# Kernel optimization log

Measured on AMD Instinct MI355X. Metric: run time of the kernel, lower is better.

Reference implementation:

```python
import jax, jax.numpy as jnp
import numpy as np

LN_EPS = 1e-5


def setup_inputs() -> dict:
    key = jax.random.key(0)
    ks = jax.random.split(key, 5)
    B, P, C, D = 8192, 25, 256, 5
    return {
        "features": jax.random.normal(ks[0], (B, P, C), dtype=jnp.float32),
        "weights": jax.random.normal(ks[1], (P, C, C), dtype=jnp.float32) * 0.05,
        "bias": jax.random.normal(ks[2], (P, C), dtype=jnp.float32) * 0.05,
        "ln_gamma": jnp.ones((C,), dtype=jnp.float32),
        "ln_beta": jnp.zeros((C,), dtype=jnp.float32),
        "lin_w": jax.random.normal(ks[3], (D, C), dtype=jnp.float32) * 0.05,
        "lin_b": jnp.zeros((D,), dtype=jnp.float32),
    }


def reference(features, weights, bias, ln_gamma, ln_beta, lin_w, lin_b):
    # Torch: (features.unsqueeze(-1) * weights).sum(-1) + bias
    # Broadcast [B,P,C,1]*[P,C,C] then sum over last axis reduces the SAME
    # broadcast axis, so it equals features * row-sums of weights (per point).
    w_rowsum = jnp.sum(weights, axis=-1)            # [P, C]
    point_wise = features * w_rowsum + bias          # [B, P, C]
    # LayerNorm over the channel dim
    mu = jnp.mean(point_wise, axis=-1, keepdims=True)
    var = jnp.mean(jnp.square(point_wise - mu), axis=-1, keepdims=True)
    pw_norm = (point_wise - mu) * jax.lax.rsqrt(var + LN_EPS)
    pw_norm = pw_norm * ln_gamma + ln_beta
    # residual + ReLU + final linear
    h = jax.nn.relu(features + pw_norm)              # [B, P, C]
    return jnp.einsum("bpc,dc->bpd", h, lin_w) + lin_b  # [B, P, D]
```

## Files before the change

kernel.cpp:

```cpp
#include <hip/hip_runtime.h>

#define LN_EPS 1e-5f

__global__ __launch_bounds__(256) void wrowsum_kernel(
    const float* __restrict__ w, float* __restrict__ wr, int n_rows) {
  const int lane = threadIdx.x & 63;
  const int wv   = threadIdx.x >> 6;
  const int rc   = blockIdx.x * 4 + wv;
  if (rc >= n_rows) return;
  const float4 v = reinterpret_cast<const float4*>(w)[(size_t)rc * 64 + lane];
  float s = v.x + v.y + v.z + v.w;
#pragma unroll
  for (int off = 32; off; off >>= 1) s += __shfl_xor(s, off);
  if (lane == 0) wr[rc] = s;
}

__global__ __launch_bounds__(256) void fused_main(
    const float* __restrict__ features,
    const float* __restrict__ wrow,
    const float* __restrict__ bias,
    const float* __restrict__ gamma,
    const float* __restrict__ beta,
    const float* __restrict__ lin_w,
    const float* __restrict__ lin_b,
    float* __restrict__ out,
    int n_rows, int P) {
  const int lane = threadIdx.x & 63;
  const int wv   = threadIdx.x >> 6;
  const int r    = blockIdx.x * 4 + wv;
  if (r >= n_rows) return;
  const int p = r % P;

  const float4 f  = reinterpret_cast<const float4*>(features)[(size_t)r * 64 + lane];
  const float4 wr = reinterpret_cast<const float4*>(wrow + (size_t)p * 256)[lane];
  const float4 bs = reinterpret_cast<const float4*>(bias + (size_t)p * 256)[lane];
  const float4 g  = reinterpret_cast<const float4*>(gamma)[lane];
  const float4 bt = reinterpret_cast<const float4*>(beta)[lane];

  const float pw0 = fmaf(f.x, wr.x, bs.x);
  const float pw1 = fmaf(f.y, wr.y, bs.y);
  const float pw2 = fmaf(f.z, wr.z, bs.z);
  const float pw3 = fmaf(f.w, wr.w, bs.w);

  float s1 = (pw0 + pw1) + (pw2 + pw3);
  float s2 = fmaf(pw0, pw0, fmaf(pw1, pw1, fmaf(pw2, pw2, pw3 * pw3)));
#pragma unroll
  for (int off = 32; off; off >>= 1) {
    s1 += __shfl_xor(s1, off);
    s2 += __shfl_xor(s2, off);
  }
  const float mu  = s1 * (1.0f / 256.0f);
  const float var = fmaf(-mu, mu, s2 * (1.0f / 256.0f));
  const float inv = rsqrtf(var + LN_EPS);

  const float h0 = fmaxf(fmaf((pw0 - mu) * inv, g.x, bt.x) + f.x, 0.0f);
  const float h1 = fmaxf(fmaf((pw1 - mu) * inv, g.y, bt.y) + f.y, 0.0f);
  const float h2 = fmaxf(fmaf((pw2 - mu) * inv, g.z, bt.z) + f.z, 0.0f);
  const float h3 = fmaxf(fmaf((pw3 - mu) * inv, g.w, bt.w) + f.w, 0.0f);

  float acc[5];
#pragma unroll
  for (int d = 0; d < 5; ++d) {
    const float4 lw = reinterpret_cast<const float4*>(lin_w + d * 256)[lane];
    acc[d] = fmaf(h0, lw.x, fmaf(h1, lw.y, fmaf(h2, lw.z, h3 * lw.w)));
  }
#pragma unroll
  for (int off = 32; off; off >>= 1) {
#pragma unroll
    for (int d = 0; d < 5; ++d) acc[d] += __shfl_xor(acc[d], off);
  }

  if (lane < 5) {
    float v;
    switch (lane) {
      case 0:  v = acc[0]; break;
      case 1:  v = acc[1]; break;
      case 2:  v = acc[2]; break;
      case 3:  v = acc[3]; break;
      default: v = acc[4]; break;
    }
    out[(size_t)r * 5 + lane] = v + lin_b[lane];
  }
}

extern "C" void kernel_launch(void* const* d_in, const int* in_sizes, int n_in,
                              void* d_out, int out_size, void* d_ws, size_t ws_size,
                              hipStream_t stream) {
  const float* features = (const float*)d_in[0];
  const float* weights  = (const float*)d_in[1];
  const float* bias     = (const float*)d_in[2];
  const float* gamma    = (const float*)d_in[3];
  const float* beta     = (const float*)d_in[4];
  const float* lin_w    = (const float*)d_in[5];
  const float* lin_b    = (const float*)d_in[6];
  float* out = (float*)d_out;

  const int C  = 256;
  const int PC = in_sizes[2];
  const int P  = PC / C;
  const int BP = in_sizes[0] / C;

  float* wr = (float*)d_ws;

  wrowsum_kernel<<<(PC + 3) / 4, 256, 0, stream>>>(weights, wr, PC);

  fused_main<<<(BP + 3) / 4, 256, 0, stream>>>(
      features, wr, bias, gamma, beta, lin_w, lin_b, out, BP, P);
}
```

Measured before the change: 325.0 us.

## Process four rows per wavefront with 16-lane subgroups and shorter reductions

Each 64-lane wavefront now handles four rows, with 16 lanes per row and each lane loading four float4 chunks. Cross-lane reductions for the LayerNorm statistics and the final linear drop from six shuffle steps to four, and the grid shrinks by four. The aim is to cut shuffle and reduction overhead and raise memory-level parallelism per thread, at the cost of more registers per thread.

```diff
diff --git a/kernel.cpp b/kernel.cpp
--- a/kernel.cpp
+++ b/kernel.cpp
@@ -27,25 +27,46 @@
     int n_rows, int P) {
   const int lane = threadIdx.x & 63;
   const int wv   = threadIdx.x >> 6;
-  const int r    = blockIdx.x * 4 + wv;
+  const int sub  = lane & 15;
+  const int rg   = lane >> 4;
+  const int r    = blockIdx.x * 16 + wv * 4 + rg;
   if (r >= n_rows) return;
   const int p = r % P;
 
-  const float4 f  = reinterpret_cast<const float4*>(features)[(size_t)r * 64 + lane];
-  const float4 wr = reinterpret_cast<const float4*>(wrow + (size_t)p * 256)[lane];
-  const float4 bs = reinterpret_cast<const float4*>(bias + (size_t)p * 256)[lane];
-  const float4 g  = reinterpret_cast<const float4*>(gamma)[lane];
-  const float4 bt = reinterpret_cast<const float4*>(beta)[lane];
+  const float4* __restrict__ f4  = reinterpret_cast<const float4*>(features);
+  const float4* __restrict__ w4  = reinterpret_cast<const float4*>(wrow);
+  const float4* __restrict__ b4  = reinterpret_cast<const float4*>(bias);
+  const float4* __restrict__ g4  = reinterpret_cast<const float4*>(gamma);
+  const float4* __restrict__ t4  = reinterpret_cast<const float4*>(beta);
+  const float4* __restrict__ l4  = reinterpret_cast<const float4*>(lin_w);
 
-  const float pw0 = fmaf(f.x, wr.x, bs.x);
-  const float pw1 = fmaf(f.y, wr.y, bs.y);
-  const float pw2 = fmaf(f.z, wr.z, bs.z);
-  const float pw3 = fmaf(f.w, wr.w, bs.w);
+  float4 f[4], wr[4], bs[4], g[4], bt[4];
+#pragma unroll
+  for (int i = 0; i < 4; ++i) {
+    const int c4 = i * 16 + sub;
+    f[i]  = f4[(size_t)r * 64 + c4];
+    wr[i] = w4[(size_t)p * 64 + c4];
+    bs[i] = b4[(size_t)p * 64 + c4];
+    g[i]  = g4[c4];
+    bt[i] = t4[c4];
+  }
 
-  float s1 = (pw0 + pw1) + (pw2 + pw3);
-  float s2 = fmaf(pw0, pw0, fmaf(pw1, pw1, fmaf(pw2, pw2, pw3 * pw3)));
+  float4 pw[4];
+  float s1 = 0.0f, s2 = 0.0f;
 #pragma unroll
-  for (int off = 32; off; off >>= 1) {
+  for (int i = 0; i < 4; ++i) {
+    pw[i].x = fmaf(f[i].x, wr[i].x, bs[i].x);
+    pw[i].y = fmaf(f[i].y, wr[i].y, bs[i].y);
+    pw[i].z = fmaf(f[i].z, wr[i].z, bs[i].z);
+    pw[i].w = fmaf(f[i].w, wr[i].w, bs[i].w);
+    s1 += (pw[i].x + pw[i].y) + (pw[i].z + pw[i].w);
+    s2 = fmaf(pw[i].x, pw[i].x, s2);
+    s2 = fmaf(pw[i].y, pw[i].y, s2);
+    s2 = fmaf(pw[i].z, pw[i].z, s2);
+    s2 = fmaf(pw[i].w, pw[i].w, s2);
+  }
+#pragma unroll
+  for (int off = 8; off; off >>= 1) {
     s1 += __shfl_xor(s1, off);
     s2 += __shfl_xor(s2, off);
   }
@@ -53,33 +74,45 @@
   const float var = fmaf(-mu, mu, s2 * (1.0f / 256.0f));
   const float inv = rsqrtf(var + LN_EPS);
 
-  const float h0 = fmaxf(fmaf((pw0 - mu) * inv, g.x, bt.x) + f.x, 0.0f);
-  const float h1 = fmaxf(fmaf((pw1 - mu) * inv, g.y, bt.y) + f.y, 0.0f);
-  const float h2 = fmaxf(fmaf((pw2 - mu) * inv, g.z, bt.z) + f.z, 0.0f);
-  const float h3 = fmaxf(fmaf((pw3 - mu) * inv, g.w, bt.w) + f.w, 0.0f);
+  float4 h[4];
+#pragma unroll
+  for (int i = 0; i < 4; ++i) {
+    h[i].x = fmaxf(fmaf((pw[i].x - mu) * inv, g[i].x, bt[i].x) + f[i].x, 0.0f);
+    h[i].y = fmaxf(fmaf((pw[i].y - mu) * inv, g[i].y, bt[i].y) + f[i].y, 0.0f);
+    h[i].z = fmaxf(fmaf((pw[i].z - mu) * inv, g[i].z, bt[i].z) + f[i].z, 0.0f);
+    h[i].w = fmaxf(fmaf((pw[i].w - mu) * inv, g[i].w, bt[i].w) + f[i].w, 0.0f);
+  }
 
   float acc[5];
 #pragma unroll
   for (int d = 0; d < 5; ++d) {
-    const float4 lw = reinterpret_cast<const float4*>(lin_w + d * 256)[lane];
-    acc[d] = fmaf(h0, lw.x, fmaf(h1, lw.y, fmaf(h2, lw.z, h3 * lw.w)));
+    float a = 0.0f;
+#pragma unroll
+    for (int i = 0; i < 4; ++i) {
+      const float4 lw = l4[d * 64 + i * 16 + sub];
+      a = fmaf(h[i].x, lw.x, a);
+      a = fmaf(h[i].y, lw.y, a);
+      a = fmaf(h[i].z, lw.z, a);
+      a = fmaf(h[i].w, lw.w, a);
+    }
+    acc[d] = a;
   }
 #pragma unroll
-  for (int off = 32; off; off >>= 1) {
+  for (int off = 8; off; off >>= 1) {
 #pragma unroll
     for (int d = 0; d < 5; ++d) acc[d] += __shfl_xor(acc[d], off);
   }
 
-  if (lane < 5) {
+  if (sub < 5) {
     float v;
-    switch (lane) {
+    switch (sub) {
       case 0:  v = acc[0]; break;
       case 1:  v = acc[1]; break;
       case 2:  v = acc[2]; break;
       case 3:  v = acc[3]; break;
       default: v = acc[4]; break;
     }
-    out[(size_t)r * 5 + lane] = v + lin_b[lane];
+    out[(size_t)r * 5 + sub] = v + lin_b[sub];
   }
 }
 
@@ -104,6 +137,6 @@
 
   wrowsum_kernel<<<(PC + 3) / 4, 256, 0, stream>>>(weights, wr, PC);
 
-  fused_main<<<(BP + 3) / 4, 256, 0, stream>>>(
+  fused_main<<<(BP + 15) / 16, 256, 0, stream>>>(
       features, wr, bias, gamma, beta, lin_w, lin_b, out, BP, P);
 }
```

After: 325.5 us. No clear change (+0.2%).
